# Performance work log

Hardware: AMD Instinct MI355X
Metric: run time of the kernel (lower is better)

Reference implementation:

```python
import jax, jax.numpy as jnp
import numpy as np

B, H, HKV, SQ, SKV, D = 2, 16, 4, 2048, 2048, 64
G = H // HKV  # query heads per kv head group
NSEG = 8


def setup_inputs() -> dict:
    key = jax.random.key(0)
    kq, kk, kv_, ks1, ks2 = jax.random.split(key, 5)
    q = jax.random.normal(kq, (B, H, SQ, D), dtype=jnp.float32)
    k = jax.random.normal(kk, (B, HKV, SKV, D), dtype=jnp.float32)
    v = jax.random.normal(kv_, (B, HKV, SKV, D), dtype=jnp.float32)
    q_segment_ids = jnp.sort(jax.random.randint(ks1, (B, SQ), 0, NSEG, dtype=jnp.int32), axis=-1)
    kv_segment_ids = jnp.sort(jax.random.randint(ks2, (B, SKV), 0, NSEG, dtype=jnp.int32), axis=-1)
    return {"q": q, "k": k, "v": v, "q_segment_ids": q_segment_ids, "kv_segment_ids": kv_segment_ids}


def reference(q, k, v, q_segment_ids, kv_segment_ids):
    # q: [B,H,SQ,D], k/v: [B,HKV,SKV,D]; GQA: each kv head serves G query heads.
    softmax_scale = 1.0 / jnp.sqrt(jnp.asarray(D, jnp.float32))
    qg = q.reshape(B, HKV, G, SQ, D)
    # scores: [B,HKV,G,SQ,SKV]
    scores = jnp.einsum("bhgsd,bhtd->bhgst", qg, k) * softmax_scale
    # segment mask: attend only within the same segment, and q_seg must be >= 0
    same_seg = (q_segment_ids[:, :, None] == kv_segment_ids[:, None, :]) & (
        q_segment_ids[:, :, None] >= 0
    )  # [B,SQ,SKV]
    mask = same_seg[:, None, None, :, :]
    masked_scores = jnp.where(mask, scores, -jnp.inf)
    m = jnp.max(masked_scores, axis=-1)  # [B,HKV,G,SQ], may be -inf for fully-masked rows
    m_safe = jnp.where(m == -jnp.inf, 0.0, m)
    p = jnp.where(mask, jnp.exp(scores - m_safe[..., None]), 0.0)
    l = jnp.sum(p, axis=-1)  # [B,HKV,G,SQ]
    acc = jnp.einsum("bhgst,bhtd->bhgsd", p, v)
    l_safe = jnp.where(l == 0.0, 1.0, l)
    out = jnp.where((l == 0.0)[..., None], 0.0, acc / l_safe[..., None])
    return out.reshape(B, H, SQ, D)
```

## Files before the change

kernel.cpp:

```cpp
#include <hip/hip_runtime.h>
#include <hip/hip_bf16.h>

#define NB   2
#define NH   16
#define NHKV 4
#define GQ   4
#define SQL  2048
#define SKV  2048
#define DH   64
#define QBLK 64
#define KVBLK 64
#define LDK  72

#define QSCALE (0.125f * 1.44269504f)
#define M2REF  (4.0f * 1.44269504f)

typedef __bf16 v8bf  __attribute__((ext_vector_type(8)));
typedef __bf16 v2bf  __attribute__((ext_vector_type(2)));
typedef float  f32x4 __attribute__((ext_vector_type(4)));
typedef unsigned u32x4 __attribute__((ext_vector_type(4)));

__global__ __launch_bounds__(256, 4)
void gqa_seg_attn(const float* __restrict__ q,
                  const float* __restrict__ k,
                  const float* __restrict__ v,
                  const int* __restrict__ qseg,
                  const int* __restrict__ kvseg,
                  float* __restrict__ out)
{
    __shared__ __bf16 k_lds[2][KVBLK][LDK];
    __shared__ __bf16 vT_lds[2][DH][LDK];
    __shared__ int    kv_start[9];

    const int tid  = threadIdx.x;
    const int lane = tid & 63;
    const int w    = tid >> 6;
    const int qt   = blockIdx.x;
    const int h    = blockIdx.y;
    const int b    = blockIdx.z;
    const int kvh  = h / GQ;
    const int q0   = qt * QBLK;

    const float* qptr   = q + (((size_t)b * NH   + h  ) * SQL) * DH;
    const float* kptr   = k + (((size_t)b * NHKV + kvh) * SKV) * DH;
    const float* vptr   = v + (((size_t)b * NHKV + kvh) * SKV) * DH;
    const int*   qsegb  = qseg  + (size_t)b * SQL;
    const int*   kvsegb = kvseg + (size_t)b * SKV;

    const int l15 = lane & 15;
    const int lg  = lane >> 4;
    const int d_a = lg * 8;

    if (tid < 9) kv_start[tid] = SKV;
    __syncthreads();
    {
        const int i0 = tid * 8;
        int prev = (tid == 0) ? -1 : kvsegb[i0 - 1];
        int4 va0 = *(const int4*)(kvsegb + i0);
        int4 va1 = *(const int4*)(kvsegb + i0 + 4);
        int vals[8] = {va0.x, va0.y, va0.z, va0.w, va1.x, va1.y, va1.z, va1.w};
        #pragma unroll
        for (int j = 0; j < 8; ++j) {
            int vv = vals[j];
            if (vv > prev)
                for (int s = prev + 1; s <= vv && s < 9; ++s) kv_start[s] = i0 + j;
            prev = vv;
        }
    }

    v8bf qfrag[2];
    {
        const int qrow = q0 + w * 16 + l15;
        for (int c = 0; c < 2; ++c) {
            const float* src = qptr + (size_t)qrow * DH + c * 32 + d_a;
            float4 f0 = *(const float4*)(src);
            float4 f1 = *(const float4*)(src + 4);
            v8bf t;
            t[0] = (__bf16)(f0.x * QSCALE); t[1] = (__bf16)(f0.y * QSCALE);
            t[2] = (__bf16)(f0.z * QSCALE); t[3] = (__bf16)(f0.w * QSCALE);
            t[4] = (__bf16)(f1.x * QSCALE); t[5] = (__bf16)(f1.y * QSCALE);
            t[6] = (__bf16)(f1.z * QSCALE); t[7] = (__bf16)(f1.w * QSCALE);
            qfrag[c] = t;
        }
    }

    __syncthreads();

    const int qsg = qsegb[q0 + w * 16 + l15];
    const int Aq  = kv_start[qsg];
    const int Bq  = kv_start[qsg + 1];

    int wlo = (Aq < Bq) ? Aq : SKV;
    int whi = (Aq < Bq) ? Bq : 0;
    for (int d = 1; d < 16; d <<= 1) {
        wlo = min(wlo, __shfl_xor(wlo, d));
        whi = max(whi, __shfl_xor(whi, d));
    }

    const int smin = qsegb[q0];
    const int smax = qsegb[q0 + QBLK - 1];
    const int lo = kv_start[smin];
    const int hi = kv_start[smax + 1];
    int t0i = lo >> 6;
    int t1i = (hi + KVBLK - 1) >> 6;
    if (hi <= lo) t1i = t0i;
    const int nt = t1i - t0i;

    const int krow = tid >> 2, kc0 = (tid & 3) * 16;
    const int kp   = tid & 31, vd0 = (tid >> 5) * 8;

    float4 ka[4], va[4];

    auto issue = [&](int kt) {
        const int kv0 = kt * KVBLK;
        const float* ks = kptr + (size_t)(kv0 + krow) * DH + kc0;
        for (int i2 = 0; i2 < 4; ++i2) ka[i2] = *(const float4*)(ks + 4 * i2);
        const float* vs0 = vptr + (size_t)(kv0 + 2 * kp) * DH + vd0;
        const float* vs1 = vs0 + DH;
        va[0] = *(const float4*)(vs0);
        va[1] = *(const float4*)(vs0 + 4);
        va[2] = *(const float4*)(vs1);
        va[3] = *(const float4*)(vs1 + 4);
    };
    auto commit = [&](int p) {
        v8bf ta, tb2;
        ta[0] = (__bf16)ka[0].x; ta[1] = (__bf16)ka[0].y;
        ta[2] = (__bf16)ka[0].z; ta[3] = (__bf16)ka[0].w;
        ta[4] = (__bf16)ka[1].x; ta[5] = (__bf16)ka[1].y;
        ta[6] = (__bf16)ka[1].z; ta[7] = (__bf16)ka[1].w;
        tb2[0] = (__bf16)ka[2].x; tb2[1] = (__bf16)ka[2].y;
        tb2[2] = (__bf16)ka[2].z; tb2[3] = (__bf16)ka[2].w;
        tb2[4] = (__bf16)ka[3].x; tb2[5] = (__bf16)ka[3].y;
        tb2[6] = (__bf16)ka[3].z; tb2[7] = (__bf16)ka[3].w;
        *(v8bf*)&k_lds[p][krow][kc0]     = ta;
        *(v8bf*)&k_lds[p][krow][kc0 + 8] = tb2;
        v2bf t;
        t[0] = (__bf16)va[0].x; t[1] = (__bf16)va[2].x; *(v2bf*)&vT_lds[p][vd0+0][2*kp] = t;
        t[0] = (__bf16)va[0].y; t[1] = (__bf16)va[2].y; *(v2bf*)&vT_lds[p][vd0+1][2*kp] = t;
        t[0] = (__bf16)va[0].z; t[1] = (__bf16)va[2].z; *(v2bf*)&vT_lds[p][vd0+2][2*kp] = t;
        t[0] = (__bf16)va[0].w; t[1] = (__bf16)va[2].w; *(v2bf*)&vT_lds[p][vd0+3][2*kp] = t;
        t[0] = (__bf16)va[1].x; t[1] = (__bf16)va[3].x; *(v2bf*)&vT_lds[p][vd0+4][2*kp] = t;
        t[0] = (__bf16)va[1].y; t[1] = (__bf16)va[3].y; *(v2bf*)&vT_lds[p][vd0+5][2*kp] = t;
        t[0] = (__bf16)va[1].z; t[1] = (__bf16)va[3].z; *(v2bf*)&vT_lds[p][vd0+6][2*kp] = t;
        t[0] = (__bf16)va[1].w; t[1] = (__bf16)va[3].w; *(v2bf*)&vT_lds[p][vd0+7][2*kp] = t;
    };

    float l_acc = 0.f;
    f32x4 o_acc[4];
    for (int t = 0; t < 4; ++t) o_acc[t] = (f32x4){0.f, 0.f, 0.f, 0.f};

    const int src0 = ((lg & 1) << 5) | l15;
    const int src1 = src0 + 16;
    const bool hi2 = (lg >= 2);

    if (nt > 0) { issue(t0i); commit(0); }

    for (int i = 0; i < nt; ++i) {
        __syncthreads();
        const int p = i & 1;
        const int kv0 = (t0i + i) * KVBLK;
        if (i + 1 < nt) issue(t0i + i + 1);

        if (!(kv0 >= whi || kv0 + KVBLK <= wlo)) {
            f32x4 s[4];
            __builtin_amdgcn_s_setprio(1);
            #pragma unroll
            for (int n = 0; n < 4; ++n) {
                s[n] = (f32x4){-M2REF, -M2REF, -M2REF, -M2REF};
                #pragma unroll
                for (int c = 0; c < 2; ++c) {
                    v8bf kb = *(const v8bf*)&k_lds[p][n * 16 + l15][c * 32 + d_a];
                    s[n] = __builtin_amdgcn_mfma_f32_16x16x32_bf16(kb, qfrag[c], s[n], 0, 0, 0);
                }
            }
            __builtin_amdgcn_s_setprio(0);

            unsigned dw[4][2];
            const int kvb = kv0 + 4 * lg;
            #pragma unroll
            for (int n = 0; n < 4; ++n) {
                float pv[4];
                #pragma unroll
                for (int r = 0; r < 4; ++r) {
                    const int kv = kvb + 16 * n + r;
                    float e = __builtin_amdgcn_exp2f(s[n][r]);
                    pv[r] = (kv >= Aq && kv < Bq) ? e : 0.f;
                    l_acc += pv[r];
                }
                v2bf pk0, pk1;
                pk0[0] = (__bf16)pv[0]; pk0[1] = (__bf16)pv[1];
                pk1[0] = (__bf16)pv[2]; pk1[1] = (__bf16)pv[3];
                dw[n][0] = __builtin_bit_cast(unsigned, pk0);
                dw[n][1] = __builtin_bit_cast(unsigned, pk1);
            }

            v8bf pa[2];
            #pragma unroll
            for (int c = 0; c < 2; ++c) {
                unsigned a0 = __shfl(dw[2*c][0],   src0), b0 = __shfl(dw[2*c+1][0], src0);
                unsigned a1 = __shfl(dw[2*c][1],   src0), b1 = __shfl(dw[2*c+1][1], src0);
                unsigned a2 = __shfl(dw[2*c][0],   src1), b2 = __shfl(dw[2*c+1][0], src1);
                unsigned a3 = __shfl(dw[2*c][1],   src1), b3 = __shfl(dw[2*c+1][1], src1);
                u32x4 x;
                x[0] = hi2 ? b0 : a0; x[1] = hi2 ? b1 : a1;
                x[2] = hi2 ? b2 : a2; x[3] = hi2 ? b3 : a3;
                pa[c] = __builtin_bit_cast(v8bf, x);
            }

            __builtin_amdgcn_s_setprio(1);
            #pragma unroll
            for (int t = 0; t < 4; ++t)
                #pragma unroll
                for (int c = 0; c < 2; ++c) {
                    v8bf vb = *(const v8bf*)&vT_lds[p][t * 16 + l15][c * 32 + d_a];
                    o_acc[t] = __builtin_amdgcn_mfma_f32_16x16x32_bf16(pa[c], vb, o_acc[t], 0, 0, 0);
                }
            __builtin_amdgcn_s_setprio(0);
        }

        if (i + 1 < nt) commit((i + 1) & 1);
    }

    float x = l_acc;
    x += __shfl_xor(x, 16);
    x += __shfl_xor(x, 32);
    const float inv = (x > 0.f) ? (1.f / x) : 0.f;

    float* outp = out + (((size_t)b * NH + h) * SQL) * DH;
    const int qrow_c0 = q0 + w * 16 + (lg << 2);
    #pragma unroll
    for (int r = 0; r < 4; ++r) {
        const float invr = __shfl(inv, 4 * lg + r);
        #pragma unroll
        for (int t = 0; t < 4; ++t)
            outp[(size_t)(qrow_c0 + r) * DH + t * 16 + l15] = o_acc[t][r] * invr;
    }
}

extern "C" void kernel_launch(void* const* d_in, const int* in_sizes, int n_in,
                              void* d_out, int out_size, void* d_ws, size_t ws_size,
                              hipStream_t stream) {
    const float* q     = (const float*)d_in[0];
    const float* k     = (const float*)d_in[1];
    const float* v     = (const float*)d_in[2];
    const int*   qseg  = (const int*)d_in[3];
    const int*   kvseg = (const int*)d_in[4];
    float* out = (float*)d_out;

    dim3 grid(SQL / QBLK, NH, NB);
    dim3 block(256);
    gqa_seg_attn<<<grid, block, 0, stream>>>(q, k, v, qseg, kvseg, out);
}
```

Baseline: 37.77 us.

## Make attention kernel persistent with per-KV-head atomic work queues

Replaces the one-block-per-query-tile grid with a persistent grid of 96 blocks per (batch, KV head) slab. Each block pulls (query head, query tile) tasks from an atomic counter in the workspace, which a small init kernel zeroes first. The kv segment start table is built once per block instead of once per tile, and tiles of different cost are balanced dynamically. The change also lowers launch-bounds occupancy from 4 to 3 and adds a second kernel launch plus atomic and barrier overhead per task.

```diff
diff --git a/kernel.cpp b/kernel.cpp
--- a/kernel.cpp
+++ b/kernel.cpp
@@ -11,6 +11,9 @@
 #define QBLK 64
 #define KVBLK 64
 #define LDK  72
+#define BLOCKS_PER_SLAB 96
+#define TASKS_PER_SLAB  (32 * GQ)
+#define NSLAB (NB * NHKV)
 
 #define QSCALE (0.125f * 1.44269504f)
 #define M2REF  (4.0f * 1.44269504f)
@@ -20,36 +23,40 @@
 typedef float  f32x4 __attribute__((ext_vector_type(4)));
 typedef unsigned u32x4 __attribute__((ext_vector_type(4)));
 
-__global__ __launch_bounds__(256, 4)
+__global__ void init_counters(unsigned* cnt) {
+    if (threadIdx.x < NSLAB) cnt[threadIdx.x] = 0u;
+}
+
+template<int PERSIST>
+__global__ __launch_bounds__(256, 3)
 void gqa_seg_attn(const float* __restrict__ q,
                   const float* __restrict__ k,
                   const float* __restrict__ v,
                   const int* __restrict__ qseg,
                   const int* __restrict__ kvseg,
-                  float* __restrict__ out)
+                  float* __restrict__ out,
+                  unsigned* __restrict__ cnt)
 {
     __shared__ __bf16 k_lds[2][KVBLK][LDK];
     __shared__ __bf16 vT_lds[2][DH][LDK];
     __shared__ int    kv_start[9];
+    __shared__ int    task_s;
 
     const int tid  = threadIdx.x;
     const int lane = tid & 63;
     const int w    = tid >> 6;
-    const int qt   = blockIdx.x;
-    const int h    = blockIdx.y;
-    const int b    = blockIdx.z;
-    const int kvh  = h / GQ;
-    const int q0   = qt * QBLK;
-
-    const float* qptr   = q + (((size_t)b * NH   + h  ) * SQL) * DH;
+    const int l15  = lane & 15;
+    const int lg   = lane >> 4;
+    const int d_a  = lg * 8;
+
+    const int kvh = PERSIST ? blockIdx.y : ((int)blockIdx.y / GQ);
+    const int b   = blockIdx.z;
+    const int slab = b * NHKV + kvh;
+
     const float* kptr   = k + (((size_t)b * NHKV + kvh) * SKV) * DH;
     const float* vptr   = v + (((size_t)b * NHKV + kvh) * SKV) * DH;
     const int*   qsegb  = qseg  + (size_t)b * SQL;
     const int*   kvsegb = kvseg + (size_t)b * SKV;
-
-    const int l15 = lane & 15;
-    const int lg  = lane >> 4;
-    const int d_a = lg * 8;
 
     if (tid < 9) kv_start[tid] = SKV;
     __syncthreads();
@@ -67,47 +74,13 @@
             prev = vv;
         }
     }
-
-    v8bf qfrag[2];
-    {
-        const int qrow = q0 + w * 16 + l15;
-        for (int c = 0; c < 2; ++c) {
-            const float* src = qptr + (size_t)qrow * DH + c * 32 + d_a;
-            float4 f0 = *(const float4*)(src);
-            float4 f1 = *(const float4*)(src + 4);
-            v8bf t;
-            t[0] = (__bf16)(f0.x * QSCALE); t[1] = (__bf16)(f0.y * QSCALE);
-            t[2] = (__bf16)(f0.z * QSCALE); t[3] = (__bf16)(f0.w * QSCALE);
-            t[4] = (__bf16)(f1.x * QSCALE); t[5] = (__bf16)(f1.y * QSCALE);
-            t[6] = (__bf16)(f1.z * QSCALE); t[7] = (__bf16)(f1.w * QSCALE);
-            qfrag[c] = t;
-        }
-    }
-
     __syncthreads();
-
-    const int qsg = qsegb[q0 + w * 16 + l15];
-    const int Aq  = kv_start[qsg];
-    const int Bq  = kv_start[qsg + 1];
-
-    int wlo = (Aq < Bq) ? Aq : SKV;
-    int whi = (Aq < Bq) ? Bq : 0;
-    for (int d = 1; d < 16; d <<= 1) {
-        wlo = min(wlo, __shfl_xor(wlo, d));
-        whi = max(whi, __shfl_xor(whi, d));
-    }
-
-    const int smin = qsegb[q0];
-    const int smax = qsegb[q0 + QBLK - 1];
-    const int lo = kv_start[smin];
-    const int hi = kv_start[smax + 1];
-    int t0i = lo >> 6;
-    int t1i = (hi + KVBLK - 1) >> 6;
-    if (hi <= lo) t1i = t0i;
-    const int nt = t1i - t0i;
 
     const int krow = tid >> 2, kc0 = (tid & 3) * 16;
     const int kp   = tid & 31, vd0 = (tid >> 5) * 8;
+    const int src0 = ((lg & 1) << 5) | l15;
+    const int src1 = src0 + 16;
+    const bool hi2 = (lg >= 2);
 
     float4 ka[4], va[4];
 
@@ -145,95 +118,147 @@
         t[0] = (__bf16)va[1].w; t[1] = (__bf16)va[3].w; *(v2bf*)&vT_lds[p][vd0+7][2*kp] = t;
     };
 
-    float l_acc = 0.f;
-    f32x4 o_acc[4];
-    for (int t = 0; t < 4; ++t) o_acc[t] = (f32x4){0.f, 0.f, 0.f, 0.f};
-
-    const int src0 = ((lg & 1) << 5) | l15;
-    const int src1 = src0 + 16;
-    const bool hi2 = (lg >= 2);
-
-    if (nt > 0) { issue(t0i); commit(0); }
-
-    for (int i = 0; i < nt; ++i) {
-        __syncthreads();
-        const int p = i & 1;
-        const int kv0 = (t0i + i) * KVBLK;
-        if (i + 1 < nt) issue(t0i + i + 1);
-
-        if (!(kv0 >= whi || kv0 + KVBLK <= wlo)) {
-            f32x4 s[4];
-            __builtin_amdgcn_s_setprio(1);
-            #pragma unroll
-            for (int n = 0; n < 4; ++n) {
-                s[n] = (f32x4){-M2REF, -M2REF, -M2REF, -M2REF};
+    for (;;) {
+        int qt, h;
+        if (PERSIST) {
+            if (tid == 0) task_s = (int)atomicAdd(&cnt[slab], 1u);
+            __syncthreads();
+            const int t = task_s;
+            if (t >= TASKS_PER_SLAB) break;
+            h  = kvh * GQ + (t >> 5);
+            qt = t & 31;
+        } else {
+            h  = blockIdx.y;
+            qt = blockIdx.x;
+        }
+        const int q0 = qt * QBLK;
+        const float* qptr = q + (((size_t)b * NH + h) * SQL) * DH;
+
+        v8bf qfrag[2];
+        {
+            const int qrow = q0 + w * 16 + l15;
+            for (int c = 0; c < 2; ++c) {
+                const float* src = qptr + (size_t)qrow * DH + c * 32 + d_a;
+                float4 f0 = *(const float4*)(src);
+                float4 f1 = *(const float4*)(src + 4);
+                v8bf t;
+                t[0] = (__bf16)(f0.x * QSCALE); t[1] = (__bf16)(f0.y * QSCALE);
+                t[2] = (__bf16)(f0.z * QSCALE); t[3] = (__bf16)(f0.w * QSCALE);
+                t[4] = (__bf16)(f1.x * QSCALE); t[5] = (__bf16)(f1.y * QSCALE);
+                t[6] = (__bf16)(f1.z * QSCALE); t[7] = (__bf16)(f1.w * QSCALE);
+                qfrag[c] = t;
+            }
+        }
+
+        const int qsg = qsegb[q0 + w * 16 + l15];
+        const int Aq  = kv_start[qsg];
+        const int Bq  = kv_start[qsg + 1];
+
+        int wlo = (Aq < Bq) ? Aq : SKV;
+        int whi = (Aq < Bq) ? Bq : 0;
+        for (int d = 1; d < 16; d <<= 1) {
+            wlo = min(wlo, __shfl_xor(wlo, d));
+            whi = max(whi, __shfl_xor(whi, d));
+        }
+
+        const int smin = qsegb[q0];
+        const int smax = qsegb[q0 + QBLK - 1];
+        const int lo = kv_start[smin];
+        const int hi = kv_start[smax + 1];
+        int t0i = lo >> 6;
+        int t1i = (hi + KVBLK - 1) >> 6;
+        if (hi <= lo) t1i = t0i;
+        const int nt = t1i - t0i;
+
+        float l_acc = 0.f;
+        f32x4 o_acc[4];
+        for (int t = 0; t < 4; ++t) o_acc[t] = (f32x4){0.f, 0.f, 0.f, 0.f};
+
+        if (nt > 0) { issue(t0i); commit(0); }
+
+        for (int i = 0; i < nt; ++i) {
+            __syncthreads();
+            const int p = i & 1;
+            const int kv0 = (t0i + i) * KVBLK;
+            if (i + 1 < nt) issue(t0i + i + 1);
+
+            if (!(kv0 >= whi || kv0 + KVBLK <= wlo)) {
+                f32x4 s[4];
+                __builtin_amdgcn_s_setprio(1);
+                #pragma unroll
+                for (int n = 0; n < 4; ++n) {
+                    s[n] = (f32x4){-M2REF, -M2REF, -M2REF, -M2REF};
+                    #pragma unroll
+                    for (int c = 0; c < 2; ++c) {
+                        v8bf kb = *(const v8bf*)&k_lds[p][n * 16 + l15][c * 32 + d_a];
+                        s[n] = __builtin_amdgcn_mfma_f32_16x16x32_bf16(kb, qfrag[c], s[n], 0, 0, 0);
+                    }
+                }
+                __builtin_amdgcn_s_setprio(0);
+
+                unsigned dw[4][2];
+                const int kvb = kv0 + 4 * lg;
+                #pragma unroll
+                for (int n = 0; n < 4; ++n) {
+                    float pv[4];
+                    #pragma unroll
+                    for (int r = 0; r < 4; ++r) {
+                        const int kv = kvb + 16 * n + r;
+                        float e = __builtin_amdgcn_exp2f(s[n][r]);
+                        pv[r] = (kv >= Aq && kv < Bq) ? e : 0.f;
+                        l_acc += pv[r];
+                    }
+                    v2bf pk0, pk1;
+                    pk0[0] = (__bf16)pv[0]; pk0[1] = (__bf16)pv[1];
+                    pk1[0] = (__bf16)pv[2]; pk1[1] = (__bf16)pv[3];
+                    dw[n][0] = __builtin_bit_cast(unsigned, pk0);
+                    dw[n][1] = __builtin_bit_cast(unsigned, pk1);
+                }
+
+                v8bf pa[2];
                 #pragma unroll
                 for (int c = 0; c < 2; ++c) {
-                    v8bf kb = *(const v8bf*)&k_lds[p][n * 16 + l15][c * 32 + d_a];
-                    s[n] = __builtin_amdgcn_mfma_f32_16x16x32_bf16(kb, qfrag[c], s[n], 0, 0, 0);
+                    unsigned a0 = __shfl(dw[2*c][0],   src0), b0 = __shfl(dw[2*c+1][0], src0);
+                    unsigned a1 = __shfl(dw[2*c][1],   src0), b1 = __shfl(dw[2*c+1][1], src0);
+                    unsigned a2 = __shfl(dw[2*c][0],   src1), b2 = __shfl(dw[2*c+1][0], src1);
+                    unsigned a3 = __shfl(dw[2*c][1],   src1), b3 = __shfl(dw[2*c+1][1], src1);
+                    u32x4 x;
+                    x[0] = hi2 ? b0 : a0; x[1] = hi2 ? b1 : a1;
+                    x[2] = hi2 ? b2 : a2; x[3] = hi2 ? b3 : a3;
+                    pa[c] = __builtin_bit_cast(v8bf, x);
                 }
+
+                __builtin_amdgcn_s_setprio(1);
+                #pragma unroll
+                for (int t = 0; t < 4; ++t)
+                    #pragma unroll
+                    for (int c = 0; c < 2; ++c) {
+                        v8bf vb = *(const v8bf*)&vT_lds[p][t * 16 + l15][c * 32 + d_a];
+                        o_acc[t] = __builtin_amdgcn_mfma_f32_16x16x32_bf16(pa[c], vb, o_acc[t], 0, 0, 0);
+                    }
+                __builtin_amdgcn_s_setprio(0);
             }
-            __builtin_amdgcn_s_setprio(0);
-
-            unsigned dw[4][2];
-            const int kvb = kv0 + 4 * lg;
-            #pragma unroll
-            for (int n = 0; n < 4; ++n) {
-                float pv[4];
-                #pragma unroll
-                for (int r = 0; r < 4; ++r) {
-                    const int kv = kvb + 16 * n + r;
-                    float e = __builtin_amdgcn_exp2f(s[n][r]);
-                    pv[r] = (kv >= Aq && kv < Bq) ? e : 0.f;
-                    l_acc += pv[r];
-                }
-                v2bf pk0, pk1;
-                pk0[0] = (__bf16)pv[0]; pk0[1] = (__bf16)pv[1];
-                pk1[0] = (__bf16)pv[2]; pk1[1] = (__bf16)pv[3];
-                dw[n][0] = __builtin_bit_cast(unsigned, pk0);
-                dw[n][1] = __builtin_bit_cast(unsigned, pk1);
-            }
-
-            v8bf pa[2];
-            #pragma unroll
-            for (int c = 0; c < 2; ++c) {
-                unsigned a0 = __shfl(dw[2*c][0],   src0), b0 = __shfl(dw[2*c+1][0], src0);
-                unsigned a1 = __shfl(dw[2*c][1],   src0), b1 = __shfl(dw[2*c+1][1], src0);
-                unsigned a2 = __shfl(dw[2*c][0],   src1), b2 = __shfl(dw[2*c+1][0], src1);
-                unsigned a3 = __shfl(dw[2*c][1],   src1), b3 = __shfl(dw[2*c+1][1], src1);
-                u32x4 x;
-                x[0] = hi2 ? b0 : a0; x[1] = hi2 ? b1 : a1;
-                x[2] = hi2 ? b2 : a2; x[3] = hi2 ? b3 : a3;
-                pa[c] = __builtin_bit_cast(v8bf, x);
-            }
-
-            __builtin_amdgcn_s_setprio(1);
+
+            if (i + 1 < nt) commit((i + 1) & 1);
+        }
+
+        float x = l_acc;
+        x += __shfl_xor(x, 16);
+        x += __shfl_xor(x, 32);
+        const float inv = (x > 0.f) ? (1.f / x) : 0.f;
+
+        float* outp = out + (((size_t)b * NH + h) * SQL) * DH;
+        const int qrow_c0 = q0 + w * 16 + (lg << 2);
+        #pragma unroll
+        for (int r = 0; r < 4; ++r) {
+            const float invr = __shfl(inv, 4 * lg + r);
             #pragma unroll
             for (int t = 0; t < 4; ++t)
-                #pragma unroll
-                for (int c = 0; c < 2; ++c) {
-                    v8bf vb = *(const v8bf*)&vT_lds[p][t * 16 + l15][c * 32 + d_a];
-                    o_acc[t] = __builtin_amdgcn_mfma_f32_16x16x32_bf16(pa[c], vb, o_acc[t], 0, 0, 0);
-                }
-            __builtin_amdgcn_s_setprio(0);
-        }
-
-        if (i + 1 < nt) commit((i + 1) & 1);
-    }
-
-    float x = l_acc;
-    x += __shfl_xor(x, 16);
-    x += __shfl_xor(x, 32);
-    const float inv = (x > 0.f) ? (1.f / x) : 0.f;
-
-    float* outp = out + (((size_t)b * NH + h) * SQL) * DH;
-    const int qrow_c0 = q0 + w * 16 + (lg << 2);
-    #pragma unroll
-    for (int r = 0; r < 4; ++r) {
-        const float invr = __shfl(inv, 4 * lg + r);
-        #pragma unroll
-        for (int t = 0; t < 4; ++t)
-            outp[(size_t)(qrow_c0 + r) * DH + t * 16 + l15] = o_acc[t][r] * invr;
+                outp[(size_t)(qrow_c0 + r) * DH + t * 16 + l15] = o_acc[t][r] * invr;
+        }
+
+        if (!PERSIST) return;
+        __syncthreads();
     }
 }
 
@@ -247,7 +272,13 @@
     const int*   kvseg = (const int*)d_in[4];
     float* out = (float*)d_out;
 
-    dim3 grid(SQL / QBLK, NH, NB);
-    dim3 block(256);
-    gqa_seg_attn<<<grid, block, 0, stream>>>(q, k, v, qseg, kvseg, out);
+    if (ws_size >= NSLAB * sizeof(unsigned)) {
+        unsigned* cnt = (unsigned*)d_ws;
+        init_counters<<<dim3(1), dim3(64), 0, stream>>>(cnt);
+        gqa_seg_attn<1><<<dim3(BLOCKS_PER_SLAB, NHKV, NB), dim3(256), 0, stream>>>(
+            q, k, v, qseg, kvseg, out, cnt);
+    } else {
+        gqa_seg_attn<0><<<dim3(32, NH, NB), dim3(256), 0, stream>>>(
+            q, k, v, qseg, kvseg, out, nullptr);
+    }
 }
```

Result: slower. 50.05 us (+32.5%).

## Map GQA head group onto block so waves share K/V tiles

Applied to the files above, without the earlier changes.

Each block now handles one KV head and a 32-row query tile, with each of the four waves taking a different query head in the group and processing two 16-row sub-tiles. K/V tiles loaded and converted into LDS are reused across all four query heads, cutting global K/V traffic and conversion work by the group factor. The per-wave skip of tiles outside the wave's segment range is removed, so some masked tiles are now computed. Register use roughly doubles (two sets of accumulators), and the occupancy hint drops from 4 to 3.

```diff
diff --git a/kernel.cpp b/kernel.cpp
--- a/kernel.cpp
+++ b/kernel.cpp
@@ -8,7 +8,7 @@
 #define SQL  2048
 #define SKV  2048
 #define DH   64
-#define QBLK 64
+#define QBLK 32
 #define KVBLK 64
 #define LDK  72
 
@@ -20,7 +20,7 @@
 typedef float  f32x4 __attribute__((ext_vector_type(4)));
 typedef unsigned u32x4 __attribute__((ext_vector_type(4)));
 
-__global__ __launch_bounds__(256, 4)
+__global__ __launch_bounds__(256, 3)
 void gqa_seg_attn(const float* __restrict__ q,
                   const float* __restrict__ k,
                   const float* __restrict__ v,
@@ -36,9 +36,9 @@
     const int lane = tid & 63;
     const int w    = tid >> 6;
     const int qt   = blockIdx.x;
-    const int h    = blockIdx.y;
+    const int kvh  = blockIdx.y;
     const int b    = blockIdx.z;
-    const int kvh  = h / GQ;
+    const int h    = kvh * GQ + w;
     const int q0   = qt * QBLK;
 
     const float* qptr   = q + (((size_t)b * NH   + h  ) * SQL) * DH;
@@ -68,11 +68,12 @@
         }
     }
 
-    v8bf qfrag[2];
-    {
-        const int qrow = q0 + w * 16 + l15;
+    v8bf qfrag[2][2];
+    #pragma unroll
+    for (int qs = 0; qs < 2; ++qs)
+        #pragma unroll
         for (int c = 0; c < 2; ++c) {
-            const float* src = qptr + (size_t)qrow * DH + c * 32 + d_a;
+            const float* src = qptr + (size_t)(q0 + qs * 16 + l15) * DH + c * 32 + d_a;
             float4 f0 = *(const float4*)(src);
             float4 f1 = *(const float4*)(src + 4);
             v8bf t;
@@ -80,21 +81,17 @@
             t[2] = (__bf16)(f0.z * QSCALE); t[3] = (__bf16)(f0.w * QSCALE);
             t[4] = (__bf16)(f1.x * QSCALE); t[5] = (__bf16)(f1.y * QSCALE);
             t[6] = (__bf16)(f1.z * QSCALE); t[7] = (__bf16)(f1.w * QSCALE);
-            qfrag[c] = t;
-        }
-    }
+            qfrag[qs][c] = t;
+        }
 
     __syncthreads();
 
-    const int qsg = qsegb[q0 + w * 16 + l15];
-    const int Aq  = kv_start[qsg];
-    const int Bq  = kv_start[qsg + 1];
-
-    int wlo = (Aq < Bq) ? Aq : SKV;
-    int whi = (Aq < Bq) ? Bq : 0;
-    for (int d = 1; d < 16; d <<= 1) {
-        wlo = min(wlo, __shfl_xor(wlo, d));
-        whi = max(whi, __shfl_xor(whi, d));
+    int Aq[2], Bq[2];
+    #pragma unroll
+    for (int qs = 0; qs < 2; ++qs) {
+        const int qsg = qsegb[q0 + qs * 16 + l15];
+        Aq[qs] = kv_start[qsg];
+        Bq[qs] = kv_start[qsg + 1];
     }
 
     const int smin = qsegb[q0];
@@ -108,6 +105,9 @@
 
     const int krow = tid >> 2, kc0 = (tid & 3) * 16;
     const int kp   = tid & 31, vd0 = (tid >> 5) * 8;
+    const int src0 = ((lg & 1) << 5) | l15;
+    const int src1 = src0 + 16;
+    const bool hi2 = (lg >= 2);
 
     float4 ka[4], va[4];
 
@@ -145,13 +145,12 @@
         t[0] = (__bf16)va[1].w; t[1] = (__bf16)va[3].w; *(v2bf*)&vT_lds[p][vd0+7][2*kp] = t;
     };
 
-    float l_acc = 0.f;
-    f32x4 o_acc[4];
-    for (int t = 0; t < 4; ++t) o_acc[t] = (f32x4){0.f, 0.f, 0.f, 0.f};
-
-    const int src0 = ((lg & 1) << 5) | l15;
-    const int src1 = src0 + 16;
-    const bool hi2 = (lg >= 2);
+    float l_acc[2] = {0.f, 0.f};
+    f32x4 o_acc[2][4];
+    #pragma unroll
+    for (int qs = 0; qs < 2; ++qs)
+        #pragma unroll
+        for (int t = 0; t < 4; ++t) o_acc[qs][t] = (f32x4){0.f, 0.f, 0.f, 0.f};
 
     if (nt > 0) { issue(t0i); commit(0); }
 
@@ -161,7 +160,8 @@
         const int kv0 = (t0i + i) * KVBLK;
         if (i + 1 < nt) issue(t0i + i + 1);
 
-        if (!(kv0 >= whi || kv0 + KVBLK <= wlo)) {
+        #pragma unroll
+        for (int qs = 0; qs < 2; ++qs) {
             f32x4 s[4];
             __builtin_amdgcn_s_setprio(1);
             #pragma unroll
@@ -170,7 +170,7 @@
                 #pragma unroll
                 for (int c = 0; c < 2; ++c) {
                     v8bf kb = *(const v8bf*)&k_lds[p][n * 16 + l15][c * 32 + d_a];
-                    s[n] = __builtin_amdgcn_mfma_f32_16x16x32_bf16(kb, qfrag[c], s[n], 0, 0, 0);
+                    s[n] = __builtin_amdgcn_mfma_f32_16x16x32_bf16(kb, qfrag[qs][c], s[n], 0, 0, 0);
                 }
             }
             __builtin_amdgcn_s_setprio(0);
@@ -184,8 +184,8 @@
                 for (int r = 0; r < 4; ++r) {
                     const int kv = kvb + 16 * n + r;
                     float e = __builtin_amdgcn_exp2f(s[n][r]);
-                    pv[r] = (kv >= Aq && kv < Bq) ? e : 0.f;
-                    l_acc += pv[r];
+                    pv[r] = (kv >= Aq[qs] && kv < Bq[qs]) ? e : 0.f;
+                    l_acc[qs] += pv[r];
                 }
                 v2bf pk0, pk1;
                 pk0[0] = (__bf16)pv[0]; pk0[1] = (__bf16)pv[1];
@@ -213,7 +213,7 @@
                 #pragma unroll
                 for (int c = 0; c < 2; ++c) {
                     v8bf vb = *(const v8bf*)&vT_lds[p][t * 16 + l15][c * 32 + d_a];
-                    o_acc[t] = __builtin_amdgcn_mfma_f32_16x16x32_bf16(pa[c], vb, o_acc[t], 0, 0, 0);
+                    o_acc[qs][t] = __builtin_amdgcn_mfma_f32_16x16x32_bf16(pa[c], vb, o_acc[qs][t], 0, 0, 0);
                 }
             __builtin_amdgcn_s_setprio(0);
         }
@@ -221,19 +221,21 @@
         if (i + 1 < nt) commit((i + 1) & 1);
     }
 
-    float x = l_acc;
-    x += __shfl_xor(x, 16);
-    x += __shfl_xor(x, 32);
-    const float inv = (x > 0.f) ? (1.f / x) : 0.f;
-
     float* outp = out + (((size_t)b * NH + h) * SQL) * DH;
-    const int qrow_c0 = q0 + w * 16 + (lg << 2);
-    #pragma unroll
-    for (int r = 0; r < 4; ++r) {
-        const float invr = __shfl(inv, 4 * lg + r);
-        #pragma unroll
-        for (int t = 0; t < 4; ++t)
-            outp[(size_t)(qrow_c0 + r) * DH + t * 16 + l15] = o_acc[t][r] * invr;
+    #pragma unroll
+    for (int qs = 0; qs < 2; ++qs) {
+        float x = l_acc[qs];
+        x += __shfl_xor(x, 16);
+        x += __shfl_xor(x, 32);
+        const float inv = (x > 0.f) ? (1.f / x) : 0.f;
+        const int qrow_c0 = q0 + qs * 16 + (lg << 2);
+        #pragma unroll
+        for (int r = 0; r < 4; ++r) {
+            const float invr = __shfl(inv, 4 * lg + r);
+            #pragma unroll
+            for (int t = 0; t < 4; ++t)
+                outp[(size_t)(qrow_c0 + r) * DH + t * 16 + l15] = o_acc[qs][t][r] * invr;
+        }
     }
 }
 
@@ -247,7 +249,7 @@
     const int*   kvseg = (const int*)d_in[4];
     float* out = (float*)d_out;
 
-    dim3 grid(SQL / QBLK, NH, NB);
+    dim3 grid(SQL / QBLK, NHKV, NB);
     dim3 block(256);
     gqa_seg_attn<<<grid, block, 0, stream>>>(q, k, v, qseg, kvseg, out);
 }
```

Result: slower. 63.93 us (+69.3%).

## Use 16x16x16 MFMA for PV so P fragments need no cross-lane shuffles

Applied to the files above, without the earlier changes.

Replaces the PV matmul's 16x16x32 bf16 MFMA with 16x16x16 MFMA, whose A-operand layout matches the score accumulator layout. The 16 cross-lane shuffles and selects that repacked P are no longer needed. The V transpose store into LDS is rewritten to write 4-wide bf16 vectors per thread instead of 2-wide. In exchange it issues twice as many MFMA instructions at half the K depth, which lowers matrix throughput per instruction, and it does more, smaller LDS reads.

```diff
diff --git a/kernel.cpp b/kernel.cpp
--- a/kernel.cpp
+++ b/kernel.cpp
@@ -16,9 +16,18 @@
 #define M2REF  (4.0f * 1.44269504f)
 
 typedef __bf16 v8bf  __attribute__((ext_vector_type(8)));
-typedef __bf16 v2bf  __attribute__((ext_vector_type(2)));
+typedef __bf16 v4bf  __attribute__((ext_vector_type(4)));
+typedef short  v4ss  __attribute__((ext_vector_type(4)));
 typedef float  f32x4 __attribute__((ext_vector_type(4)));
-typedef unsigned u32x4 __attribute__((ext_vector_type(4)));
+
+__device__ __forceinline__ f32x4 mfma16(v4bf a, v4bf b, f32x4 c) {
+#if __has_builtin(__builtin_amdgcn_mfma_f32_16x16x16_bf16)
+    return __builtin_amdgcn_mfma_f32_16x16x16_bf16(a, b, c, 0, 0, 0);
+#else
+    return __builtin_amdgcn_mfma_f32_16x16x16bf16_1k(
+        __builtin_bit_cast(v4ss, a), __builtin_bit_cast(v4ss, b), c, 0, 0, 0);
+#endif
+}
 
 __global__ __launch_bounds__(256, 4)
 void gqa_seg_attn(const float* __restrict__ q,
@@ -107,7 +116,7 @@
     const int nt = t1i - t0i;
 
     const int krow = tid >> 2, kc0 = (tid & 3) * 16;
-    const int kp   = tid & 31, vd0 = (tid >> 5) * 8;
+    const int kq   = tid & 15, dg = tid >> 4;
 
     float4 ka[4], va[4];
 
@@ -115,12 +124,8 @@
         const int kv0 = kt * KVBLK;
         const float* ks = kptr + (size_t)(kv0 + krow) * DH + kc0;
         for (int i2 = 0; i2 < 4; ++i2) ka[i2] = *(const float4*)(ks + 4 * i2);
-        const float* vs0 = vptr + (size_t)(kv0 + 2 * kp) * DH + vd0;
-        const float* vs1 = vs0 + DH;
-        va[0] = *(const float4*)(vs0);
-        va[1] = *(const float4*)(vs0 + 4);
-        va[2] = *(const float4*)(vs1);
-        va[3] = *(const float4*)(vs1 + 4);
+        const float* vs = vptr + (size_t)(kv0 + 4 * kq) * DH + 4 * dg;
+        for (int j = 0; j < 4; ++j) va[j] = *(const float4*)(vs + j * DH);
     };
     auto commit = [&](int p) {
         v8bf ta, tb2;
@@ -134,24 +139,18 @@
         tb2[6] = (__bf16)ka[3].z; tb2[7] = (__bf16)ka[3].w;
         *(v8bf*)&k_lds[p][krow][kc0]     = ta;
         *(v8bf*)&k_lds[p][krow][kc0 + 8] = tb2;
-        v2bf t;
-        t[0] = (__bf16)va[0].x; t[1] = (__bf16)va[2].x; *(v2bf*)&vT_lds[p][vd0+0][2*kp] = t;
-        t[0] = (__bf16)va[0].y; t[1] = (__bf16)va[2].y; *(v2bf*)&vT_lds[p][vd0+1][2*kp] = t;
-        t[0] = (__bf16)va[0].z; t[1] = (__bf16)va[2].z; *(v2bf*)&vT_lds[p][vd0+2][2*kp] = t;
-        t[0] = (__bf16)va[0].w; t[1] = (__bf16)va[2].w; *(v2bf*)&vT_lds[p][vd0+3][2*kp] = t;
-        t[0] = (__bf16)va[1].x; t[1] = (__bf16)va[3].x; *(v2bf*)&vT_lds[p][vd0+4][2*kp] = t;
-        t[0] = (__bf16)va[1].y; t[1] = (__bf16)va[3].y; *(v2bf*)&vT_lds[p][vd0+5][2*kp] = t;
-        t[0] = (__bf16)va[1].z; t[1] = (__bf16)va[3].z; *(v2bf*)&vT_lds[p][vd0+6][2*kp] = t;
-        t[0] = (__bf16)va[1].w; t[1] = (__bf16)va[3].w; *(v2bf*)&vT_lds[p][vd0+7][2*kp] = t;
+        #pragma unroll
+        for (int i2 = 0; i2 < 4; ++i2) {
+            v4bf wv;
+            wv[0] = (__bf16)va[0][i2]; wv[1] = (__bf16)va[1][i2];
+            wv[2] = (__bf16)va[2][i2]; wv[3] = (__bf16)va[3][i2];
+            *(v4bf*)&vT_lds[p][4 * dg + i2][4 * kq] = wv;
+        }
     };
 
     float l_acc = 0.f;
     f32x4 o_acc[4];
     for (int t = 0; t < 4; ++t) o_acc[t] = (f32x4){0.f, 0.f, 0.f, 0.f};
-
-    const int src0 = ((lg & 1) << 5) | l15;
-    const int src1 = src0 + 16;
-    const bool hi2 = (lg >= 2);
 
     if (nt > 0) { issue(t0i); commit(0); }
 
@@ -175,46 +174,32 @@
             }
             __builtin_amdgcn_s_setprio(0);
 
-            unsigned dw[4][2];
+            v4bf pfrag[4];
             const int kvb = kv0 + 4 * lg;
             #pragma unroll
             for (int n = 0; n < 4; ++n) {
-                float pv[4];
                 #pragma unroll
                 for (int r = 0; r < 4; ++r) {
                     const int kv = kvb + 16 * n + r;
                     float e = __builtin_amdgcn_exp2f(s[n][r]);
-                    pv[r] = (kv >= Aq && kv < Bq) ? e : 0.f;
-                    l_acc += pv[r];
+                    float pv = (kv >= Aq && kv < Bq) ? e : 0.f;
+                    l_acc += pv;
+                    pfrag[n][r] = (__bf16)pv;
                 }
-                v2bf pk0, pk1;
-                pk0[0] = (__bf16)pv[0]; pk0[1] = (__bf16)pv[1];
-                pk1[0] = (__bf16)pv[2]; pk1[1] = (__bf16)pv[3];
-                dw[n][0] = __builtin_bit_cast(unsigned, pk0);
-                dw[n][1] = __builtin_bit_cast(unsigned, pk1);
-            }
-
-            v8bf pa[2];
-            #pragma unroll
-            for (int c = 0; c < 2; ++c) {
-                unsigned a0 = __shfl(dw[2*c][0],   src0), b0 = __shfl(dw[2*c+1][0], src0);
-                unsigned a1 = __shfl(dw[2*c][1],   src0), b1 = __shfl(dw[2*c+1][1], src0);
-                unsigned a2 = __shfl(dw[2*c][0],   src1), b2 = __shfl(dw[2*c+1][0], src1);
-                unsigned a3 = __shfl(dw[2*c][1],   src1), b3 = __shfl(dw[2*c+1][1], src1);
-                u32x4 x;
-                x[0] = hi2 ? b0 : a0; x[1] = hi2 ? b1 : a1;
-                x[2] = hi2 ? b2 : a2; x[3] = hi2 ? b3 : a3;
-                pa[c] = __builtin_bit_cast(v8bf, x);
             }
 
             __builtin_amdgcn_s_setprio(1);
             #pragma unroll
-            for (int t = 0; t < 4; ++t)
-                #pragma unroll
-                for (int c = 0; c < 2; ++c) {
-                    v8bf vb = *(const v8bf*)&vT_lds[p][t * 16 + l15][c * 32 + d_a];
-                    o_acc[t] = __builtin_amdgcn_mfma_f32_16x16x32_bf16(pa[c], vb, o_acc[t], 0, 0, 0);
-                }
+            for (int t = 0; t < 4; ++t) {
+                v4bf vb0 = *(const v4bf*)&vT_lds[p][t * 16 + l15][0 * 16 + 4 * lg];
+                v4bf vb1 = *(const v4bf*)&vT_lds[p][t * 16 + l15][1 * 16 + 4 * lg];
+                v4bf vb2 = *(const v4bf*)&vT_lds[p][t * 16 + l15][2 * 16 + 4 * lg];
+                v4bf vb3 = *(const v4bf*)&vT_lds[p][t * 16 + l15][3 * 16 + 4 * lg];
+                o_acc[t] = mfma16(pfrag[0], vb0, o_acc[t]);
+                o_acc[t] = mfma16(pfrag[1], vb1, o_acc[t]);
+                o_acc[t] = mfma16(pfrag[2], vb2, o_acc[t]);
+                o_acc[t] = mfma16(pfrag[3], vb3, o_acc[t]);
+            }
             __builtin_amdgcn_s_setprio(0);
         }
 
```

Measured after the change: 38.01 us. Within noise of the previous version (+0.7%).
